# Optimization experiments

Measured on AMD Instinct MI355X. Metric: run time of the kernel, lower is better.

The kernel has to match this reference:

```python
import jax, jax.numpy as jnp
import numpy as np

EPS = 1e-5  # torch LayerNorm default

def setup_inputs() -> dict:
    key = jax.random.key(0)
    k1, k2, k3 = jax.random.split(key, 3)
    x = jax.random.normal(k1, (8, 256, 256, 256), dtype=jnp.float32)
    w_size = 256
    bound = 1.0 / np.sqrt(w_size)
    W = jax.random.uniform(k2, (w_size, w_size), dtype=jnp.float32, minval=-bound, maxval=bound)
    b = jax.random.uniform(k3, (w_size,), dtype=jnp.float32, minval=-bound, maxval=bound)
    return {"x": x, "W": W, "b": b}

def reference(x, W, b):
    # x: [B, 2C, G, Wd]; chunk along channel dim
    u, v = jnp.split(x, 2, axis=1)
    # LayerNorm over all non-batch dims (weight=1, bias=0 since module is
    # constructed fresh inside forward)
    mean = jnp.mean(v, axis=(1, 2, 3), keepdims=True)
    var = jnp.mean(jnp.square(v - mean), axis=(1, 2, 3), keepdims=True)
    v = (v - mean) * jax.lax.rsqrt(var + EPS)
    # Linear along last dim: y = v @ W.T + b
    v = jnp.einsum('bcgw,ow->bcgo', v, W) + b
    return u * (v + 1.0)
```

## Files before the change

### kernel.cpp

```cpp
#include <hip/hip_runtime.h>
#include <hip/hip_bf16.h>

typedef __attribute__((ext_vector_type(8))) short short8_t;
typedef __attribute__((ext_vector_type(4))) float f32x4;

__device__ __forceinline__ short f2bf(float f) {
    union { float f; unsigned u; } v; v.f = f;
    unsigned r = (v.u + 0x7FFFu + ((v.u >> 16) & 1u)) >> 16;
    return (short)r;
}

__device__ __forceinline__ f32x4 ntload4(const float* p) {
    return __builtin_nontemporal_load(reinterpret_cast<const f32x4*>(p));
}
__device__ __forceinline__ void ntstore4(float* p, f32x4 v) {
    __builtin_nontemporal_store(v, reinterpret_cast<f32x4*>(p));
}

#define N_PER_BATCH 8388608.0f
#define LDR 264

__global__ __launch_bounds__(256) void stats_partial(const float* __restrict__ x,
                                                     float2* __restrict__ partials) {
    int bid = blockIdx.x;
    int batch = bid >> 8;
    int blk   = bid & 255;
    const float* base = x + ((size_t)batch << 24) + (1u << 23) + ((size_t)blk << 15);
    int tid = threadIdx.x;
    float s1 = 0.f, s2 = 0.f;
    #pragma unroll
    for (int i = 0; i < 32; ++i) {
        float4 v = *reinterpret_cast<const float4*>(base + (size_t)(i * 256 + tid) * 4);
        s1 += v.x + v.y + v.z + v.w;
        s2 += v.x * v.x + v.y * v.y + v.z * v.z + v.w * v.w;
    }
    #pragma unroll
    for (int off = 32; off; off >>= 1) {
        s1 += __shfl_down(s1, off);
        s2 += __shfl_down(s2, off);
    }
    __shared__ float2 red[4];
    if ((tid & 63) == 0) red[tid >> 6] = make_float2(s1, s2);
    __syncthreads();
    if (tid == 0) {
        float a1 = 0.f, a2 = 0.f;
        #pragma unroll
        for (int w = 0; w < 4; ++w) { a1 += red[w].x; a2 += red[w].y; }
        partials[bid] = make_float2(a1, a2);
    }
}

__global__ __launch_bounds__(256) void stats_final(const float2* __restrict__ partials,
                                                   float2* __restrict__ stats) {
    int batch = blockIdx.x;
    int tid = threadIdx.x;
    float2 p = partials[(batch << 8) + tid];
    float s1 = p.x, s2 = p.y;
    #pragma unroll
    for (int off = 32; off; off >>= 1) {
        s1 += __shfl_down(s1, off);
        s2 += __shfl_down(s2, off);
    }
    __shared__ float2 red[4];
    if ((tid & 63) == 0) red[tid >> 6] = make_float2(s1, s2);
    __syncthreads();
    if (tid == 0) {
        float a1 = 0.f, a2 = 0.f;
        #pragma unroll
        for (int w = 0; w < 4; ++w) { a1 += red[w].x; a2 += red[w].y; }
        float mean = a1 / N_PER_BATCH;
        float var  = a2 / N_PER_BATCH - mean * mean;
        stats[batch] = make_float2(mean, rsqrtf(var + 1e-5f));
    }
}

__global__ __launch_bounds__(1024, 4) void fused_gemm(const float* __restrict__ x,
                                                      const float* __restrict__ W,
                                                      const float* __restrict__ bias,
                                                      const float2* __restrict__ stats,
                                                      float* __restrict__ out) {
    __shared__ short vt[2][16 * LDR];
    const int tid  = threadIdx.x;
    const int wid  = tid >> 6;
    const int lane = tid & 63;
    const int l15  = lane & 15;
    const int l4   = lane >> 4;
    const int q    = l15 & 3;
    const int qg   = l15 >> 2;

    short8_t bfrag[8];
    {
        const float* wbase = W + (size_t)(wid * 16 + l15) * 256 + (l4 << 3);
        #pragma unroll
        for (int kb = 0; kb < 8; ++kb) {
            float4 p0 = *reinterpret_cast<const float4*>(wbase + kb * 32);
            float4 p1 = *reinterpret_cast<const float4*>(wbase + kb * 32 + 4);
            short8_t s;
            s[0] = f2bf(p0.x); s[1] = f2bf(p0.y); s[2] = f2bf(p0.z); s[3] = f2bf(p0.w);
            s[4] = f2bf(p1.x); s[5] = f2bf(p1.y); s[6] = f2bf(p1.z); s[7] = f2bf(p1.w);
            bfrag[kb] = s;
        }
    }
    float4 bq = *reinterpret_cast<const float4*>(bias + wid * 16 + (qg << 2));
    bq.x += 1.f; bq.y += 1.f; bq.z += 1.f; bq.w += 1.f;

    const int   srow = tid >> 6;
    const int   scol = (tid & 63) << 2;
    const size_t goff = (size_t)srow * 256 + scol;
    const int   ldsw = srow * LDR + scol;

    const size_t eoff = (size_t)(l4 * 4 + q) * 256 + wid * 16 + (qg << 2);

    const int aoff = l15 * LDR + (l4 << 3);

    const int b = blockIdx.x;
    #define TILE(s) (16383 - (b + ((s) << 8)))
    #define VADDR(T) (x + ((size_t)((T) >> 11) << 24) + (1u << 23) + ((size_t)((T) & 2047) << 12))
    #define UADDR(T) (x + ((size_t)((T) >> 11) << 24) + ((size_t)((T) & 2047) << 12))

    {
        const int T0 = TILE(0);
        const float2 ms0 = stats[T0 >> 11];
        float4 v0 = *reinterpret_cast<const float4*>(VADDR(T0) + goff);
        short4 s;
        s.x = f2bf((v0.x - ms0.x) * ms0.y); s.y = f2bf((v0.y - ms0.x) * ms0.y);
        s.z = f2bf((v0.z - ms0.x) * ms0.y); s.w = f2bf((v0.w - ms0.x) * ms0.y);
        *reinterpret_cast<short4*>(&vt[0][ldsw]) = s;
    }
    const int T1i = TILE(1);
    float4 vA = *reinterpret_cast<const float4*>(VADDR(T1i) + goff);
    f32x4 uA = ntload4(UADDR(TILE(0)) + eoff);
    asm volatile("s_waitcnt lgkmcnt(0)" ::: "memory");
    __builtin_amdgcn_s_barrier();

    for (int s = 0; s < 64; ++s) {
        const int cur = s & 1;
        const int s1 = (s + 1 < 64) ? s + 1 : 63;
        const int s2 = (s + 2 < 64) ? s + 2 : 63;
        const int Ts  = TILE(s);
        const int Ts1 = TILE(s1);
        const int Ts2 = TILE(s2);

        float4 vB = *reinterpret_cast<const float4*>(VADDR(Ts2) + goff);
        f32x4 uB = ntload4(UADDR(Ts1) + eoff);
        const float2 ms1 = stats[Ts1 >> 11];

        f32x4 acc = {0.f, 0.f, 0.f, 0.f};
        #pragma unroll
        for (int kb = 0; kb < 8; ++kb) {
            short8_t a = *reinterpret_cast<const short8_t*>(&vt[cur][aoff + kb * 32]);
            acc = __builtin_amdgcn_mfma_f32_16x16x32_bf16(a, bfrag[kb], acc, 0, 0, 0);
        }

        float a0 = acc[0], a1 = acc[1], a2 = acc[2], a3 = acc[3];
        float s0 = __shfl_xor(a1, 1), s1v = __shfl_xor(a0, 1);
        float s2v = __shfl_xor(a3, 1), s3 = __shfl_xor(a2, 1);
        const bool qb0 = (q & 1);
        float w0 = qb0 ? s0 : a0;
        float w1 = qb0 ? a1 : s1v;
        float w2 = qb0 ? s2v : a2;
        float w3 = qb0 ? a3 : s3;
        float t0 = __shfl_xor(w2, 2), t1v = __shfl_xor(w3, 2);
        float t2v = __shfl_xor(w0, 2), t3 = __shfl_xor(w1, 2);
        const bool qb1 = (q & 2);
        float x0 = qb1 ? t0 : w0;
        float x1 = qb1 ? t1v : w1;
        float x2 = qb1 ? w2 : t2v;
        float x3 = qb1 ? w3 : t3;

        f32x4 o;
        o[0] = uA[0] * (x0 + bq.x);
        o[1] = uA[1] * (x1 + bq.y);
        o[2] = uA[2] * (x2 + bq.z);
        o[3] = uA[3] * (x3 + bq.w);
        ntstore4(out + ((size_t)Ts << 12) + eoff, o);

        short4 sn;
        sn.x = f2bf((vA.x - ms1.x) * ms1.y); sn.y = f2bf((vA.y - ms1.x) * ms1.y);
        sn.z = f2bf((vA.z - ms1.x) * ms1.y); sn.w = f2bf((vA.w - ms1.x) * ms1.y);
        *reinterpret_cast<short4*>(&vt[cur ^ 1][ldsw]) = sn;

        asm volatile("s_waitcnt lgkmcnt(0)" ::: "memory");
        __builtin_amdgcn_s_barrier();

        vA = vB; uA = uB;
    }
    #undef TILE
    #undef VADDR
    #undef UADDR
}

extern "C" void kernel_launch(void* const* d_in, const int* in_sizes, int n_in,
                              void* d_out, int out_size, void* d_ws, size_t ws_size,
                              hipStream_t stream) {
    const float* x    = (const float*)d_in[0];
    const float* W    = (const float*)d_in[1];
    const float* bias = (const float*)d_in[2];
    float* out = (float*)d_out;

    float2* partials = (float2*)d_ws;
    float2* stats    = (float2*)((char*)d_ws + 16384);

    stats_partial<<<2048, 256, 0, stream>>>(x, partials);
    stats_final<<<8, 256, 0, stream>>>(partials, stats);
    fused_gemm<<<256, 1024, 0, stream>>>(x, W, bias, stats, out);
}
```

Measured before the change: 184.3 us.

## Fold stats finalization into GEMM kernel and deepen u-prefetch pipeline

Removes the separate stats_final launch. Each GEMM block now reduces the 2048 partial sums for all 8 batches itself and keeps mean and rstd in shared memory. Separately, the u-tile prefetch is deepened from one to two iterations ahead, to hide more global load latency. The cost is redundant per-block reduction work, an extra barrier and more registers held per thread.

```diff
diff --git a/kernel.cpp b/kernel.cpp
--- a/kernel.cpp
+++ b/kernel.cpp
@@ -50,36 +50,14 @@
     }
 }
 
-__global__ __launch_bounds__(256) void stats_final(const float2* __restrict__ partials,
-                                                   float2* __restrict__ stats) {
-    int batch = blockIdx.x;
-    int tid = threadIdx.x;
-    float2 p = partials[(batch << 8) + tid];
-    float s1 = p.x, s2 = p.y;
-    #pragma unroll
-    for (int off = 32; off; off >>= 1) {
-        s1 += __shfl_down(s1, off);
-        s2 += __shfl_down(s2, off);
-    }
-    __shared__ float2 red[4];
-    if ((tid & 63) == 0) red[tid >> 6] = make_float2(s1, s2);
-    __syncthreads();
-    if (tid == 0) {
-        float a1 = 0.f, a2 = 0.f;
-        #pragma unroll
-        for (int w = 0; w < 4; ++w) { a1 += red[w].x; a2 += red[w].y; }
-        float mean = a1 / N_PER_BATCH;
-        float var  = a2 / N_PER_BATCH - mean * mean;
-        stats[batch] = make_float2(mean, rsqrtf(var + 1e-5f));
-    }
-}
-
 __global__ __launch_bounds__(1024, 4) void fused_gemm(const float* __restrict__ x,
                                                       const float* __restrict__ W,
                                                       const float* __restrict__ bias,
-                                                      const float2* __restrict__ stats,
+                                                      const float2* __restrict__ partials,
                                                       float* __restrict__ out) {
     __shared__ short vt[2][16 * LDR];
+    __shared__ float2 red2[16];
+    __shared__ float2 bst[8];
     const int tid  = threadIdx.x;
     const int wid  = tid >> 6;
     const int lane = tid & 63;
@@ -88,6 +66,29 @@
     const int q    = l15 & 3;
     const int qg   = l15 >> 2;
 
+    {
+        const int bb   = wid >> 1;
+        const int half = wid & 1;
+        const int li   = ((half << 6) + lane) << 1;
+        float2 p0 = partials[(bb << 8) + li];
+        float2 p1 = partials[(bb << 8) + li + 1];
+        float s1 = p0.x + p1.x, s2 = p0.y + p1.y;
+        #pragma unroll
+        for (int off = 32; off; off >>= 1) {
+            s1 += __shfl_down(s1, off);
+            s2 += __shfl_down(s2, off);
+        }
+        if (lane == 0) red2[wid] = make_float2(s1, s2);
+        __syncthreads();
+        if (tid < 8) {
+            float a1 = red2[2 * tid].x + red2[2 * tid + 1].x;
+            float a2 = red2[2 * tid].y + red2[2 * tid + 1].y;
+            float mean = a1 / N_PER_BATCH;
+            float var  = a2 / N_PER_BATCH - mean * mean;
+            bst[tid] = make_float2(mean, rsqrtf(var + 1e-5f));
+        }
+    }
+
     short8_t bfrag[8];
     {
         const float* wbase = W + (size_t)(wid * 16 + l15) * 256 + (l4 << 3);
@@ -118,32 +119,34 @@
     #define VADDR(T) (x + ((size_t)((T) >> 11) << 24) + (1u << 23) + ((size_t)((T) & 2047) << 12))
     #define UADDR(T) (x + ((size_t)((T) >> 11) << 24) + ((size_t)((T) & 2047) << 12))
 
+    __syncthreads();
+
     {
         const int T0 = TILE(0);
-        const float2 ms0 = stats[T0 >> 11];
+        const float2 ms0 = bst[T0 >> 11];
         float4 v0 = *reinterpret_cast<const float4*>(VADDR(T0) + goff);
         short4 s;
         s.x = f2bf((v0.x - ms0.x) * ms0.y); s.y = f2bf((v0.y - ms0.x) * ms0.y);
         s.z = f2bf((v0.z - ms0.x) * ms0.y); s.w = f2bf((v0.w - ms0.x) * ms0.y);
         *reinterpret_cast<short4*>(&vt[0][ldsw]) = s;
     }
-    const int T1i = TILE(1);
-    float4 vA = *reinterpret_cast<const float4*>(VADDR(T1i) + goff);
+    float4 vA = *reinterpret_cast<const float4*>(VADDR(TILE(1)) + goff);
     f32x4 uA = ntload4(UADDR(TILE(0)) + eoff);
+    f32x4 uB = ntload4(UADDR(TILE(1)) + eoff);
     asm volatile("s_waitcnt lgkmcnt(0)" ::: "memory");
     __builtin_amdgcn_s_barrier();
 
     for (int s = 0; s < 64; ++s) {
         const int cur = s & 1;
-        const int s1 = (s + 1 < 64) ? s + 1 : 63;
-        const int s2 = (s + 2 < 64) ? s + 2 : 63;
+        const int sp1 = (s + 1 < 64) ? s + 1 : 63;
+        const int sp2 = (s + 2 < 64) ? s + 2 : 63;
         const int Ts  = TILE(s);
-        const int Ts1 = TILE(s1);
-        const int Ts2 = TILE(s2);
+        const int Ts1 = TILE(sp1);
+        const int Ts2 = TILE(sp2);
 
         float4 vB = *reinterpret_cast<const float4*>(VADDR(Ts2) + goff);
-        f32x4 uB = ntload4(UADDR(Ts1) + eoff);
-        const float2 ms1 = stats[Ts1 >> 11];
+        f32x4 uC = ntload4(UADDR(Ts2) + eoff);
+        const float2 ms1 = bst[Ts1 >> 11];
 
         f32x4 acc = {0.f, 0.f, 0.f, 0.f};
         #pragma unroll
@@ -183,7 +186,7 @@
         asm volatile("s_waitcnt lgkmcnt(0)" ::: "memory");
         __builtin_amdgcn_s_barrier();
 
-        vA = vB; uA = uB;
+        vA = vB; uA = uB; uB = uC;
     }
     #undef TILE
     #undef VADDR
@@ -199,9 +202,7 @@
     float* out = (float*)d_out;
 
     float2* partials = (float2*)d_ws;
-    float2* stats    = (float2*)((char*)d_ws + 16384);
 
     stats_partial<<<2048, 256, 0, stream>>>(x, partials);
-    stats_final<<<8, 256, 0, stream>>>(partials, stats);
-    fused_gemm<<<256, 1024, 0, stream>>>(x, W, bias, stats, out);
-}
+    fused_gemm<<<256, 1024, 0, stream>>>(x, W, bias, partials, out);
+}
```

Result: no change. 184.7 us (median of 3 runs) (+0.2%).
